# Kernel tuning notes

Measured on AMD Instinct MI355X. Metric: run time of the kernel, lower is better.

The kernel has to match this reference:

```python
import jax, jax.numpy as jnp
import numpy as np
import math


def _instance_cl(z1, z2):
    # z1, z2: [B, T, C] -> per-element instance contrastive loss [B, T]
    B = z1.shape[0]
    z = jnp.concatenate([z1, z2], axis=0)          # [2B, T, C]
    z = z.transpose(1, 0, 2)                        # [T, 2B, C]
    sim = jnp.einsum('tic,tjc->tij', z, z)          # [T, 2B, 2B]
    # drop diagonal: tril(-1) shifted + triu(1) shifted -> [T, 2B, 2B-1]
    logits = jnp.tril(sim, -1)[:, :, :-1] + jnp.triu(sim, 1)[:, :, 1:]
    logits = -jax.nn.log_softmax(logits, axis=-1)
    i = jnp.arange(B)
    loss = (logits[:, i, B + i - 1] + logits[:, B + i, i]) / 2.0   # [T, B]
    return loss.T                                    # [B, T]


def _temporal_cl(z1, z2):
    # z1, z2: [B, T, C] -> per-timestep temporal contrastive loss [B, T]
    T = z1.shape[1]
    z = jnp.concatenate([z1, z2], axis=1)            # [B, 2T, C]
    sim = jnp.einsum('bic,bjc->bij', z, z)           # [B, 2T, 2T]
    logits = jnp.tril(sim, -1)[:, :, :-1] + jnp.triu(sim, 1)[:, :, 1:]
    logits = -jax.nn.log_softmax(logits, axis=-1)
    t = jnp.arange(T)
    return (logits[:, t, T + t - 1] + logits[:, T + t, t]) / 2.0   # [B, T]


def _contrastive_corr(z1, z2, alpha=0.5):
    # per-(batch, timestep) contrastive score, shape [B, L]
    return alpha * _instance_cl(z1, z2) + (1.0 - alpha) * _temporal_cl(z1, z2)


def setup_inputs() -> dict:
    key = jax.random.key(0)
    k1, k2, k3 = jax.random.split(key, 3)
    B, L, H, E = 4, 2048, 8, 64
    queries = jax.random.normal(k1, (B, L, H, E), dtype=jnp.float32)
    keys = jax.random.normal(k2, (B, L, H, E), dtype=jnp.float32)
    values = jax.random.normal(k3, (B, L, H, E), dtype=jnp.float32)
    attn_mask = jnp.zeros((1,), dtype=bool)  # unused; ProbMask is rebuilt internally
    return {"queries": queries, "keys": keys, "values": values, "attn_mask": attn_mask}


FACTOR = 1.0


def reference(queries, keys, values, attn_mask):
    B, L, H, E = queries.shape
    # S == L here so key/value slicing branch is a no-op
    corr = _contrastive_corr(queries.reshape(B, L, H * E),
                             keys.reshape(B, L, H * E))       # [B, L]
    top_k = int(FACTOR * math.log(L))                          # static (=7 for L=2048)
    _, index = jax.lax.top_k(corr.mean(axis=0), top_k)         # [K]
    corr_top = corr[:, index]                                  # [B, K]
    # scores[b,h,k,l] = corr_top[b,k] broadcast over h and l
    scores = jnp.broadcast_to(corr_top[:, None, :, None], (B, H, top_k, L))
    # ProbMask: mask future positions l > index[k] (causal for the selected queries)
    mask = jnp.arange(L)[None, :] > index[:, None]             # [K, L]
    scores = jnp.where(mask[None, None, :, :], -jnp.inf, scores)
    attn = jax.nn.softmax(scores, axis=-1)                     # [B, H, K, L]
    V = values.transpose(0, 2, 1, 3)                           # [B, H, L, D]
    context = jnp.cumsum(V, axis=2)                            # initial context (mask_flag=True)
    out = jnp.einsum('bhkl,bhld->bhkd', attn, V)               # [B, H, K, D]
    context = context.at[:, :, index, :].set(out)              # scatter update
    return context
```

## Files before the change

kernel.cpp:

```cpp
#include <hip/hip_runtime.h>
#include <math.h>


typedef __attribute__((ext_vector_type(8))) short short8;
typedef __attribute__((ext_vector_type(8))) unsigned short ushort8;
typedef __attribute__((ext_vector_type(4))) float f32x4;

typedef const __attribute__((address_space(1))) void* gas_ptr;
typedef __attribute__((address_space(3))) void* las_ptr;

#define EXP_OFF 80.0f

__device__ __forceinline__ void async_cp16(const void* g, void* l) {
  __builtin_amdgcn_global_load_lds((gas_ptr)g, (las_ptr)l, 16, 0, 0);
}

__device__ __forceinline__ unsigned short f2bf(float x) {
  union { float f; unsigned int u; } v; v.f = x;
  unsigned int r = v.u + 0x7FFFu + ((v.u >> 16) & 1u);
  return (unsigned short)(r >> 16);
}

__global__ __launch_bounds__(256) void convert_bf16_kernel(
    const float* __restrict__ Q, const float* __restrict__ K,
    unsigned short* __restrict__ Z, float* __restrict__ part) {
  int tid = blockIdx.x * 256 + threadIdx.x;
  part[tid] = 0.f;
  int row = tid >> 6;
  int c0 = (tid & 63) * 8;
  int b = row >> 12, i = row & 4095;
  const float* src = (i < 2048)
      ? Q + ((size_t)(b * 2048 + i) * 512 + c0)
      : K + ((size_t)(b * 2048 + (i - 2048)) * 512 + c0);
  float4 v0 = ((const float4*)src)[0];
  float4 v1 = ((const float4*)src)[1];
  ushort8 o;
  o[0] = f2bf(v0.x); o[1] = f2bf(v0.y); o[2] = f2bf(v0.z); o[3] = f2bf(v0.w);
  o[4] = f2bf(v1.x); o[5] = f2bf(v1.y); o[6] = f2bf(v1.z); o[7] = f2bf(v1.w);
  *(ushort8*)(Z + (size_t)row * 512 + c0) = o;
}

__global__ __launch_bounds__(512) void temporal_gemm_kernel(
    const unsigned short* __restrict__ Z, float* __restrict__ part) {
  extern __shared__ __align__(16) unsigned short smem[];
  int id = blockIdx.x;
  int x = id & 7;
  int b = x >> 1;
  int t = (id >> 3) * 2 + (x & 1);
  int cj = (int)((sqrtf(8.0f * (float)t + 1.0f) - 1.0f) * 0.5f);
  while ((cj + 1) * (cj + 2) / 2 <= t) cj++;
  while (cj * (cj + 1) / 2 > t) cj--;
  int ri = t - cj * (cj + 1) / 2;
  const unsigned short* Zb = Z + (size_t)b * 4096 * 512;

  int tid = threadIdx.x;
  int w = tid >> 6, lane = tid & 63;
  int wr = w >> 2, wc = w & 3;
  int lm = lane & 15, q = lane >> 4;
  int swz = q ^ ((lm >> 1) & 3);

  int srow = w * 16 + (lane >> 2);
  int kq = (lane & 3) ^ ((lane >> 3) & 3);
  const unsigned short* gA0 = Zb + (size_t)(ri * 256 + srow) * 512 + kq * 8;
  const unsigned short* gA1 = gA0 + (size_t)128 * 512;
  const unsigned short* gB0 = Zb + (size_t)(cj * 256 + srow) * 512 + kq * 8;
  const unsigned short* gB1 = gB0 + (size_t)128 * 512;
  int lo0 = (w * 16) * 32;
  int lo1 = (128 + w * 16) * 32;

  f32x4 acc[8][4];
#pragma unroll
  for (int mi = 0; mi < 8; mi++)
#pragma unroll
    for (int ni = 0; ni < 4; ni++) acc[mi][ni] = (f32x4)(0.f);

#define STAGE(kt_)                                                     \
  do {                                                                 \
    unsigned short* base_ = smem + (((kt_) & 3) * 16384);              \
    int go_ = (kt_) * 32;                                              \
    async_cp16(gA0 + go_, base_ + lo0);                                \
    async_cp16(gA1 + go_, base_ + lo1);                                \
    async_cp16(gB0 + go_, base_ + 8192 + lo0);                         \
    async_cp16(gB1 + go_, base_ + 8192 + lo1);                         \
  } while (0)

  STAGE(0);
  STAGE(1);
  STAGE(2);

  for (int kt = 0; kt < 16; ++kt) {
    if (kt + 3 < 16) STAGE(kt + 3);

    if (kt < 13)
      asm volatile("s_waitcnt vmcnt(12)" ::: "memory");
    else if (kt == 13)
      asm volatile("s_waitcnt vmcnt(8)" ::: "memory");
    else if (kt == 14)
      asm volatile("s_waitcnt vmcnt(4)" ::: "memory");
    else
      asm volatile("s_waitcnt vmcnt(0)" ::: "memory");
    asm volatile("s_barrier" ::: "memory");

    const unsigned short* A = smem + (kt & 3) * 16384;
    const unsigned short* B = A + 8192;
    short8 af[8], bfr[4];
#pragma unroll
    for (int mi = 0; mi < 8; mi++) {
      int ar = wr * 128 + mi * 16 + lm;
      af[mi] = *(const short8*)(A + ar * 32 + swz * 8);
    }
#pragma unroll
    for (int ni = 0; ni < 4; ni++) {
      int bc = wc * 64 + ni * 16 + lm;
      bfr[ni] = *(const short8*)(B + bc * 32 + swz * 8);
    }
    __builtin_amdgcn_s_setprio(1);
#pragma unroll
    for (int mi = 0; mi < 8; mi++)
#pragma unroll
      for (int ni = 0; ni < 4; ni++)
        acc[mi][ni] = __builtin_amdgcn_mfma_f32_16x16x32_bf16(
            af[mi], bfr[ni], acc[mi][ni], 0, 0, 0);
    __builtin_amdgcn_s_setprio(0);
    asm volatile("s_barrier" ::: "memory");
  }
#undef STAGE

  float csum[4];
#pragma unroll
  for (int ni = 0; ni < 4; ni++) csum[ni] = 0.f;

#pragma unroll
  for (int mi = 0; mi < 8; mi++) {
    float rs[4];
#pragma unroll
    for (int rr = 0; rr < 4; rr++) rs[rr] = 0.f;
#pragma unroll
    for (int ni = 0; ni < 4; ni++) {
#pragma unroll
      for (int rr = 0; rr < 4; rr++) {
        int R = ri * 256 + wr * 128 + mi * 16 + q * 4 + rr;
        int Cg = cj * 256 + wc * 64 + ni * 16 + lm;
        float e = (R != Cg) ? __expf(acc[mi][ni][rr] - EXP_OFF) : 0.f;
        rs[rr] += e;
        csum[ni] += e;
      }
    }
#pragma unroll
    for (int rr = 0; rr < 4; rr++) {
      float s = rs[rr];
      s += __shfl_xor(s, 1);
      s += __shfl_xor(s, 2);
      s += __shfl_xor(s, 4);
      s += __shfl_xor(s, 8);
      if (lm == 0) {
        int R = ri * 256 + wr * 128 + mi * 16 + q * 4 + rr;
        part[((size_t)(b * 4096 + R)) * 64 + cj * 4 + wc] = s;
      }
    }
  }

  if (ri != cj) {
#pragma unroll
    for (int ni = 0; ni < 4; ni++) {
      float s = csum[ni];
      s += __shfl_xor(s, 16);
      s += __shfl_xor(s, 32);
      if (q == 0) {
        int Cg = cj * 256 + wc * 64 + ni * 16 + lm;
        part[((size_t)(b * 4096 + Cg)) * 64 + ri * 2 + wr] = s;
      }
    }
  }
}

__global__ __launch_bounds__(256) void merge_row_kernel(
    const float* __restrict__ part, float* __restrict__ lse_temp) {
  int row = blockIdx.x * 256 + threadIdx.x;
  const float4* p = (const float4*)(part + (size_t)row * 64);
  float s = 0.f;
#pragma unroll
  for (int i = 0; i < 16; i++) {
    float4 v = p[i];
    s += v.x + v.y + v.z + v.w;
  }
  lse_temp[row] = EXP_OFF + __logf(s);
}

__global__ __launch_bounds__(256) void instance_kernel(
    const unsigned short* __restrict__ Z,
    float* __restrict__ lse_inst ,
    float* __restrict__ posdot ) {
  int wave = (blockIdx.x * 256 + threadIdx.x) >> 6;
  int t0 = wave * 2;
  int lane = threadIdx.x & 63;
  int lm = lane & 15, q = lane >> 4;
  int tt = (lm < 8) ? t0 : t0 + 1;
  int v = lm & 7;
  size_t zrow = (v < 4) ? ((size_t)v * 4096 + tt)
                        : ((size_t)(v - 4) * 4096 + 2048 + tt);
  const unsigned short* g = Z + zrow * 512 + q * 8;

  f32x4 acc0 = (f32x4)(0.f), acc1 = (f32x4)(0.f);
#pragma unroll
  for (int kc = 0; kc < 16; kc += 2) {
    short8 a0 = *(const short8*)(g + kc * 32);
    short8 a1 = *(const short8*)(g + kc * 32 + 32);
    acc0 = __builtin_amdgcn_mfma_f32_16x16x32_bf16(a0, a0, acc0, 0, 0, 0);
    acc1 = __builtin_amdgcn_mfma_f32_16x16x32_bf16(a1, a1, acc1, 0, 0, 0);
  }
  f32x4 acc = acc0 + acc1;

#pragma unroll
  for (int rr = 0; rr < 4; rr++) {
    int i = q * 4 + rr;
    float val = acc[rr];
    bool samehalf = ((i < 8) == (lm < 8));
    int t = (i < 8) ? t0 : t0 + 1;
    int iv = i & 7;
    if (samehalf && iv < 4 && (lm & 7) == iv + 4)
      posdot[iv * 2048 + t] = val;
    float dd = (samehalf && lm != i) ? val : -INFINITY;
    float mt = dd;
    mt = fmaxf(mt, __shfl_xor(mt, 1));
    mt = fmaxf(mt, __shfl_xor(mt, 2));
    mt = fmaxf(mt, __shfl_xor(mt, 4));
    float e = __expf(dd - mt);
    e += __shfl_xor(e, 1);
    e += __shfl_xor(e, 2);
    e += __shfl_xor(e, 4);
    if ((lm & 7) == 0 && samehalf) lse_inst[t * 8 + iv] = mt + __logf(e);
  }
}

__global__ __launch_bounds__(256) void combine_topk_kernel(
    const float* __restrict__ lse_inst, const float* __restrict__ lse_temp,
    const float* __restrict__ posdot, int* __restrict__ index_out) {
  __shared__ float wmax[4];
  __shared__ int widx[4];
  int tid = threadIdx.x;
  int base = tid * 8;
  float v[8];
#pragma unroll
  for (int r = 0; r < 8; r++) {
    int t = base + r;
    float sum = 0.f;
#pragma unroll
    for (int b = 0; b < 4; b++) {
      sum += 0.25f * (lse_inst[t * 8 + b] + lse_inst[t * 8 + 4 + b] +
                      lse_temp[b * 4096 + t] + lse_temp[b * 4096 + 2048 + t]) -
             posdot[b * 2048 + t];
    }
    v[r] = sum * 0.25f;
  }
  int lane = tid & 63, w = tid >> 6;
  for (int k = 0; k < 7; k++) {
    float bv = v[0];
    int bi = base;
#pragma unroll
    for (int r = 1; r < 8; r++)
      if (v[r] > bv) { bv = v[r]; bi = base + r; }
#pragma unroll
    for (int d = 1; d < 64; d <<= 1) {
      float ov = __shfl_xor(bv, d);
      int oi = __shfl_xor(bi, d);
      if (ov > bv || (ov == bv && oi < bi)) { bv = ov; bi = oi; }
    }
    if (lane == 0) { wmax[w] = bv; widx[w] = bi; }
    __syncthreads();
    float BV = wmax[0];
    int BI = widx[0];
#pragma unroll
    for (int ww = 1; ww < 4; ww++)
      if (wmax[ww] > BV || (wmax[ww] == BV && widx[ww] < BI)) {
        BV = wmax[ww];
        BI = widx[ww];
      }
    if (tid == 0) index_out[k] = BI;
    if (BI >= base && BI < base + 8) v[BI - base] = -INFINITY;
    __syncthreads();
  }
}

__global__ __launch_bounds__(64) void cumsum_psum_kernel(
    const float* __restrict__ V, float* __restrict__ psum) {
  int gb = blockIdx.x;
  int bh = gb >> 6, g = gb & 63;
  int h = bh & 7, b = bh >> 3;
  int lane = threadIdx.x;
  int ro = lane >> 4, e4 = (lane & 15) * 4;
  const float* base =
      V + (size_t)(b * 2048 + g * 32 + ro) * 512 + h * 64 + e4;
  float sx = 0.f, sy = 0.f, sz = 0.f, sw = 0.f;
#pragma unroll
  for (int k = 0; k < 8; k++) {
    float4 v = *(const float4*)(base + (size_t)(k * 4) * 512);
    sx += v.x; sy += v.y; sz += v.z; sw += v.w;
  }
  sx += __shfl_xor(sx, 16); sy += __shfl_xor(sy, 16);
  sz += __shfl_xor(sz, 16); sw += __shfl_xor(sw, 16);
  sx += __shfl_xor(sx, 32); sy += __shfl_xor(sy, 32);
  sz += __shfl_xor(sz, 32); sw += __shfl_xor(sw, 32);
  if (ro == 0) {
    float4 o = {sx, sy, sz, sw};
    *(float4*)(psum + ((size_t)bh * 64 + g) * 64 + e4) = o;
  }
}

__global__ __launch_bounds__(256) void cumsum_write_kernel(
    const float* __restrict__ V, const float* __restrict__ psum,
    const int* __restrict__ index, float* __restrict__ out) {
  int blk = blockIdx.x;
  int bh = blk >> 4, chunk = blk & 15;
  int h = bh & 7, b = bh >> 3;
  int tid = threadIdx.x;
  int e = tid & 63, sub = tid >> 6;
  int g = chunk * 4 + sub;

  const float* ps = psum + (size_t)bh * 64 * 64;
  float run = 0.f;
  for (int gg = 0; gg < g; ++gg) run += ps[gg * 64 + e];

  int idx[7];
#pragma unroll
  for (int k = 0; k < 7; k++) idx[k] = index[k];

  const float* Vbase = V + (size_t)(b * 2048) * 512 + h * 64 + e;
  float* obase = out + (size_t)bh * 2048 * 64 + e;

  int l0 = g * 32;
#pragma unroll 4
  for (int l = l0; l < l0 + 32; ++l) {
    run += Vbase[(size_t)l * 512];
    float o = run;
    bool special = false;
#pragma unroll
    for (int k = 0; k < 7; k++) special = special || (idx[k] == l);
    if (special) o = run / (float)(l + 1);
    obase[(size_t)l * 64] = o;
  }
}

extern "C" void kernel_launch(void* const* d_in, const int* in_sizes, int n_in,
                              void* d_out, int out_size, void* d_ws, size_t ws_size,
                              hipStream_t stream) {
  const float* Q = (const float*)d_in[0];
  const float* K = (const float*)d_in[1];
  const float* V = (const float*)d_in[2];
  float* out = (float*)d_out;

  unsigned short* Z = (unsigned short*)d_ws;
  float* base = (float*)d_ws + 4 * 4096 * 512 / 2;
  float* part = base;
  float* lse_t = base + 4 * 4096 * 64;
  float* lse_i = lse_t + 16384;
  float* posd = lse_i + 16384;
  int* idx = (int*)(posd + 8192);
  float* psum = part;

  static bool attr_set = false;
  if (!attr_set) {
    hipFuncSetAttribute((const void*)temporal_gemm_kernel,
                        hipFuncAttributeMaxDynamicSharedMemorySize, 131072);
    attr_set = true;
  }

  convert_bf16_kernel<<<4096, 256, 0, stream>>>(Q, K, Z, part);
  temporal_gemm_kernel<<<544, 512, 131072, stream>>>(Z, part);
  instance_kernel<<<256, 256, 0, stream>>>(Z, lse_i, posd);
  merge_row_kernel<<<64, 256, 0, stream>>>(part, lse_t);
  combine_topk_kernel<<<1, 256, 0, stream>>>(lse_i, lse_t, posd, idx);
  cumsum_psum_kernel<<<2048, 64, 0, stream>>>(V, psum);
  cumsum_write_kernel<<<512, 256, 0, stream>>>(V, psum, idx, out);
}
```

Before: 207.6 us.

## Restructure GEMM mainloop into 8-phase ping-pong schedule with interleaved async loads

Replaces the 4-stage K-tile pipeline (32-wide K steps, 16 iterations) with a double-buffered schedule using 64-wide K tiles. Each iteration is split into 8 phases that interleave small global-to-LDS copies with LDS fragment reads and MFMA groups, and uses fine-grained barriers and vmcnt waits. The aim is to overlap memory traffic with matrix math and to cut loop and barrier overhead per MFMA. It adds many more barriers per iteration and relies on intricate buffer indexing and wait counts, which could introduce races or stalls if any of them are wrong.

```diff
diff --git a/kernel.cpp b/kernel.cpp
--- a/kernel.cpp
+++ b/kernel.cpp
@@ -61,12 +61,12 @@
 
   int srow = w * 16 + (lane >> 2);
   int kq = (lane & 3) ^ ((lane >> 3) & 3);
-  const unsigned short* gA0 = Zb + (size_t)(ri * 256 + srow) * 512 + kq * 8;
-  const unsigned short* gA1 = gA0 + (size_t)128 * 512;
-  const unsigned short* gB0 = Zb + (size_t)(cj * 256 + srow) * 512 + kq * 8;
-  const unsigned short* gB1 = gB0 + (size_t)128 * 512;
-  int lo0 = (w * 16) * 32;
-  int lo1 = (128 + w * 16) * 32;
+  const unsigned short* gA = Zb + (size_t)(ri * 256 + srow) * 512 + kq * 8;
+  const unsigned short* gB = Zb + (size_t)(cj * 256 + srow) * 512 + kq * 8;
+
+  const unsigned short* abase = smem + wr * 8192 + lm * 32 + swz * 8;
+  const unsigned short* bbase =
+      smem + 16384 + (wc >> 1) * 8192 + ((wc & 1) * 64 + lm) * 32 + swz * 8;
 
   f32x4 acc[8][4];
 #pragma unroll
@@ -74,57 +74,79 @@
 #pragma unroll
     for (int ni = 0; ni < 4; ni++) acc[mi][ni] = (f32x4)(0.f);
 
-#define STAGE(kt_)                                                     \
-  do {                                                                 \
-    unsigned short* base_ = smem + (((kt_) & 3) * 16384);              \
-    int go_ = (kt_) * 32;                                              \
-    async_cp16(gA0 + go_, base_ + lo0);                                \
-    async_cp16(gA1 + go_, base_ + lo1);                                \
-    async_cp16(gB0 + go_, base_ + 8192 + lo0);                         \
-    async_cp16(gB1 + go_, base_ + 8192 + lo1);                         \
+#define STG(gbase, matoff, kt, h)                                          \
+  do {                                                                     \
+    const unsigned short* s_ =                                             \
+        (gbase) + (size_t)(h) * 65536 + (((kt) & 7) * 64);                 \
+    unsigned short* d_ =                                                   \
+        smem + (((kt) & 1) * 32768) + (matoff) + (h) * 8192 + w * 512;     \
+    async_cp16(s_, d_);                                        \
+    async_cp16(s_ + 32, d_ + 4096);                            \
   } while (0)
 
-  STAGE(0);
-  STAGE(1);
-  STAGE(2);
-
-  for (int kt = 0; kt < 16; ++kt) {
-    if (kt + 3 < 16) STAGE(kt + 3);
-
-    if (kt < 13)
-      asm volatile("s_waitcnt vmcnt(12)" ::: "memory");
-    else if (kt == 13)
-      asm volatile("s_waitcnt vmcnt(8)" ::: "memory");
-    else if (kt == 14)
-      asm volatile("s_waitcnt vmcnt(4)" ::: "memory");
-    else
-      asm volatile("s_waitcnt vmcnt(0)" ::: "memory");
-    asm volatile("s_barrier" ::: "memory");
-
-    const unsigned short* A = smem + (kt & 3) * 16384;
-    const unsigned short* B = A + 8192;
-    short8 af[8], bfr[4];
-#pragma unroll
-    for (int mi = 0; mi < 8; mi++) {
-      int ar = wr * 128 + mi * 16 + lm;
-      af[mi] = *(const short8*)(A + ar * 32 + swz * 8);
-    }
-#pragma unroll
-    for (int ni = 0; ni < 4; ni++) {
-      int bc = wc * 64 + ni * 16 + lm;
-      bfr[ni] = *(const short8*)(B + bc * 32 + swz * 8);
-    }
-    __builtin_amdgcn_s_setprio(1);
-#pragma unroll
-    for (int mi = 0; mi < 8; mi++)
-#pragma unroll
-      for (int ni = 0; ni < 4; ni++)
-        acc[mi][ni] = __builtin_amdgcn_mfma_f32_16x16x32_bf16(
-            af[mi], bfr[ni], acc[mi][ni], 0, 0, 0);
-    __builtin_amdgcn_s_setprio(0);
-    asm volatile("s_barrier" ::: "memory");
-  }
-#undef STAGE
+  STG(gA, 0, 0, 0);
+  STG(gA, 0, 0, 1);
+  STG(gB, 16384, 0, 0);
+  STG(gB, 16384, 0, 1);
+  STG(gB, 16384, 1, 0);
+  STG(gB, 16384, 1, 1);
+  asm volatile("s_waitcnt vmcnt(4)" ::: "memory");
+  asm volatile("s_barrier" ::: "memory");
+
+  short8 bfr[4][2];
+
+  for (int it = 0; it < 4; ++it) {
+    int kt0 = 2 * it, kt1 = 2 * it + 1;
+#pragma unroll
+    for (int ph = 0; ph < 8; ++ph) {
+      const int s = ph >> 2;
+      const int mi0 = (ph & 3) * 2;
+      if ((ph & 3) == 0) {
+#pragma unroll
+        for (int ni = 0; ni < 4; ni++)
+#pragma unroll
+          for (int kh = 0; kh < 2; kh++)
+            bfr[ni][kh] = *(const short8*)(bbase + s * 32768 + kh * 4096 +
+                                           ni * 512);
+      }
+      short8 a00 = *(const short8*)(abase + s * 32768 + 0 * 4096 + mi0 * 512);
+      short8 a01 = *(const short8*)(abase + s * 32768 + 1 * 4096 + mi0 * 512);
+      short8 a10 =
+          *(const short8*)(abase + s * 32768 + 0 * 4096 + (mi0 + 1) * 512);
+      short8 a11 =
+          *(const short8*)(abase + s * 32768 + 1 * 4096 + (mi0 + 1) * 512);
+      switch (ph) {
+        case 0: STG(gA, 0, kt1, 0); break;
+        case 1: STG(gA, 0, kt1, 1); break;
+        case 2: STG(gB, 16384, kt0 + 2, 0); break;
+        case 3: STG(gB, 16384, kt0 + 2, 1); break;
+        case 4: STG(gA, 0, kt0 + 2, 0); break;
+        case 5: STG(gA, 0, kt0 + 2, 1); break;
+        case 6: STG(gB, 16384, kt1 + 2, 0); break;
+        case 7: STG(gB, 16384, kt1 + 2, 1); break;
+      }
+      asm volatile("s_barrier" ::: "memory");
+      asm volatile("s_waitcnt lgkmcnt(0)" ::: "memory");
+      __builtin_amdgcn_s_setprio(1);
+#pragma unroll
+      for (int ni = 0; ni < 4; ni++) {
+        acc[mi0][ni] = __builtin_amdgcn_mfma_f32_16x16x32_bf16(
+            a00, bfr[ni][0], acc[mi0][ni], 0, 0, 0);
+        acc[mi0][ni] = __builtin_amdgcn_mfma_f32_16x16x32_bf16(
+            a01, bfr[ni][1], acc[mi0][ni], 0, 0, 0);
+        acc[mi0 + 1][ni] = __builtin_amdgcn_mfma_f32_16x16x32_bf16(
+            a10, bfr[ni][0], acc[mi0 + 1][ni], 0, 0, 0);
+        acc[mi0 + 1][ni] = __builtin_amdgcn_mfma_f32_16x16x32_bf16(
+            a11, bfr[ni][1], acc[mi0 + 1][ni], 0, 0, 0);
+      }
+      __builtin_amdgcn_s_setprio(0);
+      if ((ph & 3) == 3)
+        asm volatile("s_waitcnt vmcnt(4)" ::: "memory");
+      asm volatile("s_barrier" ::: "memory");
+    }
+  }
+#undef STG
+  asm volatile("s_waitcnt vmcnt(0)" ::: "memory");
 
   float csum[4];
 #pragma unroll
```

After: 199.9 us. 3.7% less time.
